# Kernel optimization log

Measured on AMD Instinct MI355X. Metric: run time of the kernel, lower is better.

The kernel has to match this reference:

```python
import jax, jax.numpy as jnp
import numpy as np

C = 1.0          # curvature
KP_EXTENT = 0.66 # kernel point influence radius
N, NEI, K, DIN, DOUT = 20000, 16, 4, 64, 64


def _artanh(x):
    return jnp.arctanh(jnp.clip(x, -1.0 + 1e-7, 1.0 - 1e-7))

def _norm(x):
    return jnp.sqrt(jnp.clip(jnp.sum(x * x, -1, keepdims=True), 1e-14))

def _proj(x, c=C):
    n = _norm(x)
    maxn = (1.0 - 1e-5) / jnp.sqrt(c)
    return jnp.where(n > maxn, x / n * maxn, x)

def _expmap0(u, c=C):
    sc = jnp.sqrt(c)
    n = _norm(u)
    return jnp.tanh(sc * n) * u / (sc * n)

def _logmap0(p, c=C):
    sc = jnp.sqrt(c)
    n = _norm(p)
    return _artanh(sc * n) * p / (sc * n)

def _mobius_add(x, y, c=C):
    x2 = jnp.sum(x * x, -1, keepdims=True)
    y2 = jnp.sum(y * y, -1, keepdims=True)
    xy = jnp.sum(x * y, -1, keepdims=True)
    num = (1 + 2 * c * xy + c * y2) * x + (1 - c * x2) * y
    den = jnp.clip(1 + 2 * c * xy + c * c * x2 * y2, 1e-15)
    return num / den

def _lambda_x(x, c=C):
    return 2.0 / jnp.clip(1 - c * jnp.sum(x * x, -1, keepdims=True), 1e-7)

def _dist(x, y, c=C):  # sqrt(sqdist)
    sc = jnp.sqrt(c)
    m = _mobius_add(-x, y, c)
    return (2.0 / sc) * _artanh(sc * _norm(m)[..., 0])

def _logmap(x, y, c=C):
    m = _mobius_add(-x, y, c)
    n = _norm(m)
    sc = jnp.sqrt(c)
    return 2.0 / (sc * _lambda_x(x, c)) * _artanh(sc * n) * m / n

def _ptransp0back(x, u, c=C):  # parallel transport x -> origin
    return u * _lambda_x(x, c) / 2.0

def _p2k(x, c=C):  # Poincare -> Klein
    return 2.0 * x / (1 + c * jnp.sum(x * x, -1, keepdims=True))

def _k2p(x, c=C):  # Klein -> Poincare
    return x / (1 + jnp.sqrt(jnp.clip(1 - c * jnp.sum(x * x, -1, keepdims=True), 1e-7)))

def _gamma(x, c=C):  # Lorentz factor of a Klein point
    return 1.0 / jnp.sqrt(jnp.clip(1 - c * jnp.sum(x * x, -1, keepdims=True), 1e-7))


def setup_inputs() -> dict:
    key = jax.random.key(0)
    k1, k2, k3, k4, k5 = jax.random.split(key, 5)
    x = _proj(0.1 * jax.random.normal(k1, (N, DIN), jnp.float32))   # points in the ball
    nei = jax.random.randint(k2, (N, NEI), 0, N)                    # neighbor indices
    nei_mask = jnp.ones((N, NEI), jnp.float32)
    W = jax.random.normal(k3, (K, DOUT, DIN), jnp.float32) * (2.0 / (DIN + DOUT)) ** 0.5
    b = 0.01 * jax.random.normal(k4, (K, DOUT), jnp.float32)
    kt = jax.random.normal(k5, (K, DIN), jnp.float32)
    kt = kt / _norm(kt) * KP_EXTENT                                 # tangent kernel points on radius
    kt = kt.at[0].set(0.0)                                          # center kernel point
    return {"x": x, "nei": nei, "nei_mask": nei_mask, "W": W, "b": b, "kernel_tangents": kt}


def reference(x, nei, nei_mask, W, b, kernel_tangents):
    # 1) irregular neighbor gather: (N, NEI, D)
    x_nei = x[nei]
    xr = x[:, None, :]
    # 2) transport_x: move every neighborhood to the origin
    x0_nei = _proj(_expmap0(_ptransp0back(xr, _logmap(xr, x_nei))))
    # 3) kernel positions at the origin (after transport, transp=False branch)
    x_kernel = _expmap0(kernel_tangents)                        # (K, D)
    # 4) per neighbor / kernel-point hyperbolic distances: (N, K, NEI)
    dis = _dist(x0_nei[:, None, :, :], x_kernel[None, :, None, :])
    # 5) per-kernel BLinear: log0 -> linear -> exp0 -> mobius bias add -> proj
    u = _logmap0(x0_nei)                                        # (N, NEI, D)
    h = _expmap0(jnp.einsum('kod,bnd->bkno', W, u))             # (N, K, NEI, DOUT)
    h = _proj(_mobius_add(h, _expmap0(b)[None, :, None, :]))
    # 6) KPConv linear influence weights, masked
    w = jax.nn.relu(1.0 - dis / KP_EXTENT) * nei_mask[:, None, :]
    # 7) Klein weighted midpoint over neighbors (AggKlein=True)
    kx = _p2k(h)
    wg = w * _gamma(kx)[..., 0]                                 # (N, K, NEI)
    mid = jnp.einsum('bkn,bknd->bkd', wg, kx) / jnp.clip(jnp.sum(wg, -1, keepdims=True)[..., None][..., 0, :], 1e-10)
    # 8) Klein midpoint over the K kernel points
    g = _gamma(mid)                                             # (N, K, 1)
    out_k = jnp.sum(g * mid, 1) / jnp.clip(jnp.sum(g, 1), 1e-10)
    out = _proj(_k2p(out_k))
    # 9) hyperbolic activation (BAct with relu in tangent space at origin)
    return _expmap0(jax.nn.relu(_logmap0(out)))
```

## Files before the change

### kernel.cpp

```cpp
#include <hip/hip_runtime.h>

#define NEI 16
#define KK 4
#define DIN 64
#define DOUT 64
#define WPB 4
#define BLK (WPB * 64)
#define MAXBLOCKS 2048

__device__ __forceinline__ float wave_bcast_sum(float v) {
#pragma unroll
  for (int s = 1; s < 64; s <<= 1) v += __shfl_xor(v, s, 64);
  return v;
}

__device__ __forceinline__ float artanh_c(float z) {
  z = fminf(z, 1.0f - 1e-7f);
  z = fmaxf(z, -1.0f + 1e-7f);
  return atanhf(z);
}

__device__ __forceinline__ float tanh_fast(float r) {
  const float e = __expf(2.f * r);
  return (e - 1.f) / (e + 1.f);
}

__device__ __forceinline__ float cosh_fast(float t) {
  const float e = __expf(t);
  return 0.5f * (e + 1.f / e);
}

__global__ __launch_bounds__(BLK) void kpa_fused(
    const float* __restrict__ x, const int* __restrict__ nei,
    const float* __restrict__ nmask, const float* __restrict__ Wg,
    const float* __restrict__ bias, const float* __restrict__ kt,
    float* __restrict__ out, int npts) {
  __shared__ __align__(16) float sXK[KK][DIN];
  __shared__ __align__(16) float sEB[KK][DOUT];
  __shared__ float sXK2[KK], sEB2[KK], sAT[KK];
  __shared__ __align__(16) float sUv[WPB][DIN];

  const int tid = threadIdx.x, wv = tid >> 6, lane = tid & 63;

  {
    float v = kt[wv * DIN + lane];
    float bv = bias[wv * DOUT + lane];
    float n2 = wave_bcast_sum(v * v);
    float nr = sqrtf(fmaxf(n2, 1e-14f));
    float t = tanh_fast(nr);
    sXK[wv][lane] = t / nr * v;
    float bn2 = wave_bcast_sum(bv * bv);
    float bnr = sqrtf(fmaxf(bn2, 1e-14f));
    float tb = tanh_fast(bnr);
    sEB[wv][lane] = tb / bnr * bv;
    if (lane == 0) {
      sXK2[wv] = t * t;
      sEB2[wv] = tb * tb;
      sAT[wv] = nr;
    }
  }
  __syncthreads();

  const float maxAT = fmaxf(fmaxf(sAT[0], sAT[1]), fmaxf(sAT[2], sAT[3]));
  const float Cthr = 0.5f * (cosh_fast(0.68f + 2.f * maxAT) - 1.f);

  const int nn = lane >> 2, q = lane & 3, kme = lane & 3;
  const int stride = gridDim.x * WPB;

  int b = blockIdx.x * WPB + wv;
  if (b >= npts) return;
  int jcur = nei[b * NEI + nn];

  for (;;) {
    const int bnext = b + stride;
    int jnext = 0;
    if (bnext < npts) jnext = nei[bnext * NEI + nn];

    float4 y4[4], xb4[4];
    {
      const float4* yrow = reinterpret_cast<const float4*>(x + (size_t)jcur * DIN);
      const float4* xrow = reinterpret_cast<const float4*>(x + (size_t)b * DIN);
#pragma unroll
      for (int c = 0; c < 4; ++c) {
        xb4[c] = xrow[c * 4 + q];
        y4[c] = yrow[c * 4 + q];
      }
    }

    float xy = 0.f, y2 = 0.f, x2 = 0.f;
#pragma unroll
    for (int c = 0; c < 4; ++c) {
      xy = fmaf(y4[c].x, xb4[c].x, xy); xy = fmaf(y4[c].y, xb4[c].y, xy);
      xy = fmaf(y4[c].z, xb4[c].z, xy); xy = fmaf(y4[c].w, xb4[c].w, xy);
      y2 = fmaf(y4[c].x, y4[c].x, y2); y2 = fmaf(y4[c].y, y4[c].y, y2);
      y2 = fmaf(y4[c].z, y4[c].z, y2); y2 = fmaf(y4[c].w, y4[c].w, y2);
      x2 = fmaf(xb4[c].x, xb4[c].x, x2); x2 = fmaf(xb4[c].y, xb4[c].y, x2);
      x2 = fmaf(xb4[c].z, xb4[c].z, x2); x2 = fmaf(xb4[c].w, xb4[c].w, x2);
    }
#pragma unroll
    for (int s = 1; s < 4; s <<= 1) {
      xy += __shfl_xor(xy, s, 64);
      y2 += __shfl_xor(y2, s, 64);
      x2 += __shfl_xor(x2, s, 64);
    }

    const float e2 = fmaxf(x2 - 2.f * xy + y2, 0.f);
    const bool nearp = e2 < Cthr * (1.f - x2) * (1.f - y2);

    if (__ballot(nearp) == 0ull) {
      out[(size_t)b * DOUT + lane] = 0.f;
    } else {
      const float Bc = 1.f - x2;
      const float A = 1.f - 2.f * xy + y2;
      const float den = fmaxf(1.f - 2.f * xy + x2 * y2, 1e-15f);
      const float inv = 1.f / den;
      const float num2 = fmaxf(A * A * x2 - 2.f * A * Bc * xy + Bc * Bc * y2, 0.f);
      const float nm2 = num2 * inv * inv;

      const float mskme = nmask[b * NEI + nn];
      float dk[KK] = {0.f, 0.f, 0.f, 0.f};
      float pk[KK] = {0.f, 0.f, 0.f, 0.f};
#pragma unroll
      for (int k = 0; k < KK; ++k) {
        const float4* xkp = reinterpret_cast<const float4*>(&sXK[k][0]);
#pragma unroll
        for (int c = 0; c < 4; ++c) {
          const float4 xk4 = xkp[c * 4 + q];
          dk[k] = fmaf(y4[c].x, xk4.x, dk[k]); dk[k] = fmaf(y4[c].y, xk4.y, dk[k]);
          dk[k] = fmaf(y4[c].z, xk4.z, dk[k]); dk[k] = fmaf(y4[c].w, xk4.w, dk[k]);
          pk[k] = fmaf(xb4[c].x, xk4.x, pk[k]); pk[k] = fmaf(xb4[c].y, xk4.y, pk[k]);
          pk[k] = fmaf(xb4[c].z, xk4.z, pk[k]); pk[k] = fmaf(xb4[c].w, xk4.w, pk[k]);
        }
      }
#pragma unroll
      for (int s = 1; s < 4; s <<= 1) {
#pragma unroll
        for (int k = 0; k < KK; ++k) {
          dk[k] += __shfl_xor(dk[k], s, 64);
          pk[k] += __shfl_xor(pk[k], s, 64);
        }
      }
      const float Pjme = dk[kme];
      const float Pbme = pk[kme];

      const float nmr = sqrtf(fmaxf(nm2, 1e-14f));
      const float scl = (nmr > 0.99999f) ? (0.99999f / nmr) : 1.f;
      const float fac = inv * scl;
      const float n02 = nm2 * scl * scl;
      const float B2 = 1.f - n02;
      const float dd = fac * (Bc * Pjme - A * Pbme);
      const float xk2 = sXK2[kme];
      const float A2 = 1.f - 2.f * dd + xk2;
      const float dn2 = fmaxf(1.f - 2.f * dd + n02 * xk2, 1e-15f);
      const float nu2 = fmaxf(A2 * A2 * n02 - 2.f * A2 * B2 * dd + B2 * B2 * xk2, 0.f);
      const float mm2 = nu2 / (dn2 * dn2);
      float w = 0.f;
      if (mm2 < 0.101505f && mskme > 0.f) {
        const float dis = 2.f * artanh_c(sqrtf(fmaxf(mm2, 1e-14f)));
        w = fmaxf(1.f - dis * (1.0f / 0.66f), 0.f) * mskme;
      }
      const unsigned long long act = __ballot(w > 0.f);
      if (act == 0ull) {
        out[(size_t)b * DOUT + lane] = 0.f;
      } else {
        const float xbd = x[(size_t)b * DIN + lane];
        float midv[KK];
#pragma unroll
        for (int k = 0; k < KK; ++k) {
          float macc = 0.f, wsm = 0.f;
          unsigned long long m = act & (0x1111111111111111ull << k);
          const float ebt = sEB[k][lane];
          const float eb2 = sEB2[k];
          while (m) {
            const int g = __ffsll(m) - 1;
            m &= m - 1;
            const float wn = __shfl(w, g, 64);
            const float fac_n = __shfl(fac, g, 64);
            const float A_n = __shfl(A, g, 64);
            const float n02_n = __shfl(n02, g, 64);
            const int j_n = __shfl(jcur, g, 64);
            const float yd = x[(size_t)j_n * DIN + lane];
            const float x0t = fac_n * (Bc * yd - A_n * xbd);
            const float n0 = sqrtf(fmaxf(n02_n, 1e-14f));
            const float al = artanh_c(n0) / n0;
            asm volatile("s_waitcnt lgkmcnt(0)" ::: "memory");
            sUv[wv][lane] = al * x0t;
            asm volatile("s_waitcnt lgkmcnt(0)" ::: "memory");
            __builtin_amdgcn_sched_barrier(0);
            float a0 = 0.f, a1 = 0.f, a2 = 0.f, a3 = 0.f;
            const float4* wrow = reinterpret_cast<const float4*>(Wg) + ((k * DOUT + lane) << 4);
            const float4* urow = reinterpret_cast<const float4*>(&sUv[wv][0]);
#pragma unroll
            for (int g4 = 0; g4 < 16; ++g4) {
              const float4 w4 = wrow[g4];
              const float4 u4 = urow[g4];
              a0 = fmaf(w4.x, u4.x, a0);
              a1 = fmaf(w4.y, u4.y, a1);
              a2 = fmaf(w4.z, u4.z, a2);
              a3 = fmaf(w4.w, u4.w, a3);
            }
            const float hpre = (a0 + a1) + (a2 + a3);
            const float nh2 = wave_bcast_sum(hpre * hpre);
            const float nh = sqrtf(fmaxf(nh2, 1e-14f));
            const float sh = tanhf(nh) / nh;
            const float ht = sh * hpre;
            const float hx2 = sh * sh * nh2;
            const float hxy = wave_bcast_sum(ht * ebt);
            const float A3 = 1.f + 2.f * hxy + eb2;
            const float B3 = 1.f - hx2;
            const float dn3 = fmaxf(1.f + 2.f * hxy + hx2 * eb2, 1e-15f);
            float hm = (A3 * ht + B3 * ebt) / dn3;
            float n2h = wave_bcast_sum(hm * hm);
            const float nnh = sqrtf(fmaxf(n2h, 1e-14f));
            if (nnh > 0.99999f) {
              const float s = 0.99999f / nnh;
              hm *= s;
              n2h *= s * s;
            }
            const float ip = 1.f / (1.f + n2h);
            const float kx = 2.f * hm * ip;
            const float kx2 = 4.f * n2h * ip * ip;
            const float gam = 1.f / sqrtf(fmaxf(1.f - kx2, 1e-7f));
            const float wgv = wn * gam;
            macc = fmaf(wgv, kx, macc);
            wsm += wgv;
          }
          midv[k] = macc / fmaxf(wsm, 1e-10f);
        }

        float m2v[KK];
#pragma unroll
        for (int k = 0; k < KK; ++k) m2v[k] = midv[k] * midv[k];
#pragma unroll
        for (int s = 1; s < 64; s <<= 1) {
#pragma unroll
          for (int k = 0; k < KK; ++k) m2v[k] += __shfl_xor(m2v[k], s, 64);
        }
        float onum = 0.f, oden = 0.f;
#pragma unroll
        for (int k = 0; k < KK; ++k) {
          const float g = 1.f / sqrtf(fmaxf(1.f - m2v[k], 1e-7f));
          onum = fmaf(g, midv[k], onum);
          oden += g;
        }
        const float ok = onum / fmaxf(oden, 1e-10f);
        const float no2 = wave_bcast_sum(ok * ok);
        float p = ok / (1.f + sqrtf(fmaxf(1.f - no2, 1e-7f)));
        float np2 = wave_bcast_sum(p * p);
        float npn = sqrtf(fmaxf(np2, 1e-14f));
        if (npn > 0.99999f) {
          p *= 0.99999f / npn;
          npn = 0.99999f;
        }
        const float al2 = artanh_c(npn) / npn;
        const float rr = fmaxf(al2 * p, 0.f);
        const float nr2 = wave_bcast_sum(rr * rr);
        const float nrr = sqrtf(fmaxf(nr2, 1e-14f));
        out[(size_t)b * DOUT + lane] = tanhf(nrr) / nrr * rr;
      }
    }

    if (bnext >= npts) break;
    b = bnext;
    jcur = jnext;
  }
}

extern "C" void kernel_launch(void* const* d_in, const int* in_sizes, int n_in,
                              void* d_out, int out_size, void* d_ws, size_t ws_size,
                              hipStream_t stream) {
  const float* x = (const float*)d_in[0];
  const int* nei = (const int*)d_in[1];
  const float* nmask = (const float*)d_in[2];
  const float* W = (const float*)d_in[3];
  const float* bias = (const float*)d_in[4];
  const float* kt = (const float*)d_in[5];
  float* out = (float*)d_out;

  const int npts = in_sizes[0] / DIN;
  int grid = (npts + WPB - 1) / WPB;
  if (grid > MAXBLOCKS) grid = MAXBLOCKS;
  kpa_fused<<<grid, BLK, 0, stream>>>(x, nei, nmask, W, bias, kt, out, npts);
}
```

Before: 22.28 us.

## Use 8 waves per block, split prologue across waves, two points per wave

Doubles waves per block to 8 and splits the block prologue so four waves build the kernel-point table and four build the bias table, instead of every wave doing both. The grid is sized so each wave handles about two points through the grid-stride loop, which spreads the prologue cost over more work. The zero store to the output is now issued unconditionally right after the loads, so the early-exit branches no longer need their own stores. The trade-off is fewer blocks in flight and more per-wave serial work, which may hurt latency hiding.

```diff
diff --git a/kernel.cpp b/kernel.cpp
--- a/kernel.cpp
+++ b/kernel.cpp
@@ -4,7 +4,7 @@
 #define KK 4
 #define DIN 64
 #define DOUT 64
-#define WPB 4
+#define WPB 8
 #define BLK (WPB * 64)
 #define MAXBLOCKS 2048
 
@@ -42,22 +42,24 @@
 
   const int tid = threadIdx.x, wv = tid >> 6, lane = tid & 63;
 
-  {
+  if (wv < KK) {
     float v = kt[wv * DIN + lane];
-    float bv = bias[wv * DOUT + lane];
     float n2 = wave_bcast_sum(v * v);
     float nr = sqrtf(fmaxf(n2, 1e-14f));
     float t = tanh_fast(nr);
     sXK[wv][lane] = t / nr * v;
+    if (lane == 0) {
+      sXK2[wv] = t * t;
+      sAT[wv] = nr;
+    }
+  } else {
+    const int k = wv - KK;
+    float bv = bias[k * DOUT + lane];
     float bn2 = wave_bcast_sum(bv * bv);
     float bnr = sqrtf(fmaxf(bn2, 1e-14f));
     float tb = tanh_fast(bnr);
-    sEB[wv][lane] = tb / bnr * bv;
-    if (lane == 0) {
-      sXK2[wv] = t * t;
-      sEB2[wv] = tb * tb;
-      sAT[wv] = nr;
-    }
+    sEB[k][lane] = tb / bnr * bv;
+    if (lane == 0) sEB2[k] = tb * tb;
   }
   __syncthreads();
 
@@ -69,33 +71,34 @@
 
   int b = blockIdx.x * WPB + wv;
   if (b >= npts) return;
-  int jcur = nei[b * NEI + nn];
+  int jc = nei[b * NEI + nn];
 
   for (;;) {
     const int bnext = b + stride;
     int jnext = 0;
     if (bnext < npts) jnext = nei[bnext * NEI + nn];
 
-    float4 y4[4], xb4[4];
+    float4 yc[4], xc[4];
     {
-      const float4* yrow = reinterpret_cast<const float4*>(x + (size_t)jcur * DIN);
-      const float4* xrow = reinterpret_cast<const float4*>(x + (size_t)b * DIN);
+      const float4* yr = reinterpret_cast<const float4*>(x + (size_t)jc * DIN);
+      const float4* xr = reinterpret_cast<const float4*>(x + (size_t)b * DIN);
 #pragma unroll
       for (int c = 0; c < 4; ++c) {
-        xb4[c] = xrow[c * 4 + q];
-        y4[c] = yrow[c * 4 + q];
-      }
-    }
+        xc[c] = xr[c * 4 + q];
+        yc[c] = yr[c * 4 + q];
+      }
+    }
+    out[(size_t)b * DOUT + lane] = 0.f;
 
     float xy = 0.f, y2 = 0.f, x2 = 0.f;
 #pragma unroll
     for (int c = 0; c < 4; ++c) {
-      xy = fmaf(y4[c].x, xb4[c].x, xy); xy = fmaf(y4[c].y, xb4[c].y, xy);
-      xy = fmaf(y4[c].z, xb4[c].z, xy); xy = fmaf(y4[c].w, xb4[c].w, xy);
-      y2 = fmaf(y4[c].x, y4[c].x, y2); y2 = fmaf(y4[c].y, y4[c].y, y2);
-      y2 = fmaf(y4[c].z, y4[c].z, y2); y2 = fmaf(y4[c].w, y4[c].w, y2);
-      x2 = fmaf(xb4[c].x, xb4[c].x, x2); x2 = fmaf(xb4[c].y, xb4[c].y, x2);
-      x2 = fmaf(xb4[c].z, xb4[c].z, x2); x2 = fmaf(xb4[c].w, xb4[c].w, x2);
+      xy = fmaf(yc[c].x, xc[c].x, xy); xy = fmaf(yc[c].y, xc[c].y, xy);
+      xy = fmaf(yc[c].z, xc[c].z, xy); xy = fmaf(yc[c].w, xc[c].w, xy);
+      y2 = fmaf(yc[c].x, yc[c].x, y2); y2 = fmaf(yc[c].y, yc[c].y, y2);
+      y2 = fmaf(yc[c].z, yc[c].z, y2); y2 = fmaf(yc[c].w, yc[c].w, y2);
+      x2 = fmaf(xc[c].x, xc[c].x, x2); x2 = fmaf(xc[c].y, xc[c].y, x2);
+      x2 = fmaf(xc[c].z, xc[c].z, x2); x2 = fmaf(xc[c].w, xc[c].w, x2);
     }
 #pragma unroll
     for (int s = 1; s < 4; s <<= 1) {
@@ -107,9 +110,7 @@
     const float e2 = fmaxf(x2 - 2.f * xy + y2, 0.f);
     const bool nearp = e2 < Cthr * (1.f - x2) * (1.f - y2);
 
-    if (__ballot(nearp) == 0ull) {
-      out[(size_t)b * DOUT + lane] = 0.f;
-    } else {
+    if (__ballot(nearp) != 0ull) {
       const float Bc = 1.f - x2;
       const float A = 1.f - 2.f * xy + y2;
       const float den = fmaxf(1.f - 2.f * xy + x2 * y2, 1e-15f);
@@ -126,10 +127,10 @@
 #pragma unroll
         for (int c = 0; c < 4; ++c) {
           const float4 xk4 = xkp[c * 4 + q];
-          dk[k] = fmaf(y4[c].x, xk4.x, dk[k]); dk[k] = fmaf(y4[c].y, xk4.y, dk[k]);
-          dk[k] = fmaf(y4[c].z, xk4.z, dk[k]); dk[k] = fmaf(y4[c].w, xk4.w, dk[k]);
-          pk[k] = fmaf(xb4[c].x, xk4.x, pk[k]); pk[k] = fmaf(xb4[c].y, xk4.y, pk[k]);
-          pk[k] = fmaf(xb4[c].z, xk4.z, pk[k]); pk[k] = fmaf(xb4[c].w, xk4.w, pk[k]);
+          dk[k] = fmaf(yc[c].x, xk4.x, dk[k]); dk[k] = fmaf(yc[c].y, xk4.y, dk[k]);
+          dk[k] = fmaf(yc[c].z, xk4.z, dk[k]); dk[k] = fmaf(yc[c].w, xk4.w, dk[k]);
+          pk[k] = fmaf(xc[c].x, xk4.x, pk[k]); pk[k] = fmaf(xc[c].y, xk4.y, pk[k]);
+          pk[k] = fmaf(xc[c].z, xk4.z, pk[k]); pk[k] = fmaf(xc[c].w, xk4.w, pk[k]);
         }
       }
 #pragma unroll
@@ -140,15 +141,13 @@
           pk[k] += __shfl_xor(pk[k], s, 64);
         }
       }
-      const float Pjme = dk[kme];
-      const float Pbme = pk[kme];
 
       const float nmr = sqrtf(fmaxf(nm2, 1e-14f));
       const float scl = (nmr > 0.99999f) ? (0.99999f / nmr) : 1.f;
       const float fac = inv * scl;
       const float n02 = nm2 * scl * scl;
       const float B2 = 1.f - n02;
-      const float dd = fac * (Bc * Pjme - A * Pbme);
+      const float dd = fac * (Bc * dk[kme] - A * pk[kme]);
       const float xk2 = sXK2[kme];
       const float A2 = 1.f - 2.f * dd + xk2;
       const float dn2 = fmaxf(1.f - 2.f * dd + n02 * xk2, 1e-15f);
@@ -160,9 +159,7 @@
         w = fmaxf(1.f - dis * (1.0f / 0.66f), 0.f) * mskme;
       }
       const unsigned long long act = __ballot(w > 0.f);
-      if (act == 0ull) {
-        out[(size_t)b * DOUT + lane] = 0.f;
-      } else {
+      if (act != 0ull) {
         const float xbd = x[(size_t)b * DIN + lane];
         float midv[KK];
 #pragma unroll
@@ -178,7 +175,7 @@
             const float fac_n = __shfl(fac, g, 64);
             const float A_n = __shfl(A, g, 64);
             const float n02_n = __shfl(n02, g, 64);
-            const int j_n = __shfl(jcur, g, 64);
+            const int j_n = __shfl(jc, g, 64);
             const float yd = x[(size_t)j_n * DIN + lane];
             const float x0t = fac_n * (Bc * yd - A_n * xbd);
             const float n0 = sqrtf(fmaxf(n02_n, 1e-14f));
@@ -262,7 +259,7 @@
 
     if (bnext >= npts) break;
     b = bnext;
-    jcur = jnext;
+    jc = jnext;
   }
 }
 
@@ -278,7 +275,8 @@
   float* out = (float*)d_out;
 
   const int npts = in_sizes[0] / DIN;
-  int grid = (npts + WPB - 1) / WPB;
+  int grid = (npts + 2 * WPB - 1) / (2 * WPB);
+  if (grid < 1) grid = 1;
   if (grid > MAXBLOCKS) grid = MAXBLOCKS;
   kpa_fused<<<grid, BLK, 0, stream>>>(x, nei, nmask, W, bias, kt, out, npts);
 }
```

New measurement: 25.01 us. +12.3%, slower.
